# Performance work log

Hardware: AMD Instinct MI355X
Metric: run time of the kernel (lower is better)

The kernel has to match this reference:

```python
import jax, jax.numpy as jnp
import numpy as np

D_MODEL = 768
NUM_HEADS = 12
HEAD_DIM = D_MODEL // NUM_HEADS
THETA = 10000.0
BATCH = 4
SEQ = 2048


def setup_inputs() -> dict:
    key = jax.random.key(0)
    ks = jax.random.split(key, 5)
    scale = 1.0 / np.sqrt(D_MODEL)
    x = jax.random.normal(ks[0], (BATCH, SEQ, D_MODEL), dtype=jnp.float32)
    w_q = jax.random.normal(ks[1], (D_MODEL, D_MODEL), dtype=jnp.float32) * scale
    w_k = jax.random.normal(ks[2], (D_MODEL, D_MODEL), dtype=jnp.float32) * scale
    w_v = jax.random.normal(ks[3], (D_MODEL, D_MODEL), dtype=jnp.float32) * scale
    w_o = jax.random.normal(ks[4], (D_MODEL, D_MODEL), dtype=jnp.float32) * scale
    token_positions = jnp.arange(SEQ, dtype=jnp.int32)
    return {"x": x, "w_q": w_q, "w_k": w_k, "w_v": w_v, "w_o": w_o,
            "token_positions": token_positions}


def _rope(t, positions):
    # t: [b, h, s, d]; rotate even/odd pairs with theta^(-2i/d) frequencies
    d = t.shape[-1]
    inv_freq = THETA ** (-jnp.arange(0, d, 2, dtype=jnp.float32) / d)  # [d/2]
    ang = positions.astype(jnp.float32)[:, None] * inv_freq[None, :]   # [s, d/2]
    cos, sin = jnp.cos(ang), jnp.sin(ang)
    t_even, t_odd = t[..., 0::2], t[..., 1::2]
    out_even = t_even * cos - t_odd * sin
    out_odd = t_even * sin + t_odd * cos
    return jnp.stack([out_even, out_odd], axis=-1).reshape(t.shape)


def reference(x, w_q, w_k, w_v, w_o, token_positions):
    b, s, d = x.shape
    # fused QKV projection: x @ concat(Wq, Wk, Wv).T
    w_qkv = jnp.concatenate([w_q, w_k, w_v], axis=0)  # [3d, d]
    qkv = x @ w_qkv.T                                  # [b, s, 3d]
    q, k, v = jnp.split(qkv, 3, axis=-1)
    def split_heads(t):
        return t.reshape(b, s, NUM_HEADS, HEAD_DIM).transpose(0, 2, 1, 3)  # [b,h,s,dh]
    q, k, v = split_heads(q), split_heads(k), split_heads(v)
    q = _rope(q, token_positions)
    k = _rope(k, token_positions)
    scores = jnp.einsum('bhqd,bhkd->bhqk', q, k) / np.sqrt(HEAD_DIM)  # [b,h,s,s]
    causal = jnp.tril(jnp.ones((s, s), dtype=bool))
    scores = jnp.where(causal, scores, -jnp.inf)
    attn = jax.nn.softmax(scores, axis=-1)
    out = jnp.einsum('bhqk,bhkd->bhqd', attn, v)       # [b,h,s,dh]
    out = out.transpose(0, 2, 1, 3).reshape(b, s, d)   # [b,s,d]
    return out @ w_o.T
```

## Files before the change

kernel.cpp:

```cpp
#include <hip/hip_runtime.h>
#include <hip/hip_bf16.h>
#include <math.h>

#define L2E 1.44269504088896340736f

using f32x4  = __attribute__((ext_vector_type(4))) float;
using f32x16 = __attribute__((ext_vector_type(16))) float;
using bf16x8 = __attribute__((ext_vector_type(8))) short;

static __device__ __forceinline__ float b2f(unsigned short u) {
  union { unsigned u; float f; } v; v.u = ((unsigned)u) << 16; return v.f;
}
static __device__ __forceinline__ unsigned short f2b(float f) {
  union { float f; unsigned u; } v; v.f = f;
  unsigned r = (v.u + 0x7FFFu + ((v.u >> 16) & 1u)) >> 16;
  return (unsigned short)r;
}
static __device__ __forceinline__ unsigned cvtpk(float a, float b) {
  unsigned r;
  asm("v_cvt_pk_bf16_f32 %0, %1, %2" : "=v"(r) : "v"(a), "v"(b));
  return r;
}
static __device__ __forceinline__ void plswap(unsigned& a, unsigned& b) {
#if __has_builtin(__builtin_amdgcn_permlane32_swap)
  typedef unsigned u32x2 __attribute__((ext_vector_type(2)));
  u32x2 r = __builtin_amdgcn_permlane32_swap(a, b, false, false);
  a = r[0]; b = r[1];
#else
  unsigned as = (unsigned)__shfl_xor((int)a, 32, 64);
  unsigned bs = (unsigned)__shfl_xor((int)b, 32, 64);
  bool lo = (threadIdx.x & 32) == 0;
  unsigned na = lo ? a : bs;
  unsigned nb = lo ? as : b;
  a = na; b = nb;
#endif
}

__global__ void cvt_kernel(const float* __restrict__ src,
                           unsigned short* __restrict__ dst, int n4) {
  int i = blockIdx.x * blockDim.x + threadIdx.x;
  int stride = gridDim.x * blockDim.x;
  for (; i < n4; i += stride) {
    float4 v = ((const float4*)src)[i];
    ushort4 o;
    o.x = f2b(v.x); o.y = f2b(v.y); o.z = f2b(v.z); o.w = f2b(v.w);
    ((ushort4*)dst)[i] = o;
  }
}

__global__ void rope_table_kernel(const int* __restrict__ pos,
                                  float2* __restrict__ tab) {
  int t = blockIdx.x * blockDim.x + threadIdx.x;
  int s = t >> 5, j = t & 31;
  double p = (double)pos[s];
  double freq = pow(10000.0, -(double)(2 * j) / 64.0);
  double ang = p * freq;
  tab[t] = make_float2((float)cos(ang), (float)sin(ang));
}

template <typename OUT>
__global__ __launch_bounds__(256) void gemm_nt(const unsigned short* __restrict__ A,
                                               const unsigned short* __restrict__ B,
                                               OUT* __restrict__ C,
                                               int M, int N, int K) {
  __shared__ unsigned short As[128 * 64];
  __shared__ unsigned short Bs[128 * 64];
  const int t = threadIdx.x;
  const int lane = t & 63;
  const int row_l = lane & 15;
  const int grp = lane >> 4;
  const int wave = t >> 6;
  const int wm = (wave >> 1) * 64;
  const int wn = (wave & 1) * 64;
  const int m0 = blockIdx.y * 128;
  const int n0 = blockIdx.x * 128;

  f32x4 acc[4][4];
#pragma unroll
  for (int i = 0; i < 4; ++i)
#pragma unroll
    for (int j = 0; j < 4; ++j) acc[i][j] = (f32x4){0.f, 0.f, 0.f, 0.f};

  const int srow = t >> 3;
  const int scolb = (t & 7) * 16;
  const size_t lda = (size_t)K * 2;
  const char* Ab = (const char*)A + (size_t)m0 * lda + scolb;
  const char* Bb = (const char*)B + (size_t)n0 * lda + scolb;

  for (int k0 = 0; k0 < K; k0 += 64) {
#pragma unroll
    for (int it = 0; it < 4; ++it) {
      int row = it * 32 + srow;
      const char* ga = Ab + (size_t)row * lda + (size_t)k0 * 2;
      const char* gb = Bb + (size_t)row * lda + (size_t)k0 * 2;
      __builtin_amdgcn_global_load_lds(
          (const __attribute__((address_space(1))) unsigned*)ga,
          (__attribute__((address_space(3))) unsigned*)((char*)As + it * 4096 + t * 16),
          16, 0, 0);
      __builtin_amdgcn_global_load_lds(
          (const __attribute__((address_space(1))) unsigned*)gb,
          (__attribute__((address_space(3))) unsigned*)((char*)Bs + it * 4096 + t * 16),
          16, 0, 0);
    }
    __syncthreads();
#pragma unroll
    for (int kk = 0; kk < 2; ++kk) {
      bf16x8 a[4], b[4];
#pragma unroll
      for (int i = 0; i < 4; ++i)
        a[i] = *(const bf16x8*)&As[(wm + 16 * i + row_l) * 64 + kk * 32 + grp * 8];
#pragma unroll
      for (int j = 0; j < 4; ++j)
        b[j] = *(const bf16x8*)&Bs[(wn + 16 * j + row_l) * 64 + kk * 32 + grp * 8];
#pragma unroll
      for (int i = 0; i < 4; ++i)
#pragma unroll
        for (int j = 0; j < 4; ++j)
          acc[i][j] = __builtin_amdgcn_mfma_f32_16x16x32_bf16(a[i], b[j], acc[i][j], 0, 0, 0);
    }
    __syncthreads();
  }
#pragma unroll
  for (int i = 0; i < 4; ++i)
#pragma unroll
    for (int j = 0; j < 4; ++j)
#pragma unroll
      for (int r = 0; r < 4; ++r) {
        int rowg = m0 + wm + 16 * i + grp * 4 + r;
        int colg = n0 + wn + 16 * j + row_l;
        float v = acc[i][j][r];
        if constexpr (sizeof(OUT) == 2) {
          C[(size_t)rowg * N + colg] = (OUT)f2b(v);
        } else {
          C[(size_t)rowg * N + colg] = v;
        }
      }
}

__global__ __launch_bounds__(256) void split_rope_kernel(
    const unsigned short* __restrict__ qkv, const float2* __restrict__ tab,
    unsigned short* __restrict__ Qo, unsigned short* __restrict__ Ko) {
  int idx = blockIdx.x * 256 + threadIdx.x;
  int d2 = idx & 31;
  int h = (idx >> 5) % 12;
  int m = idx / 384;
  int b = m >> 11, s = m & 2047;
  const unsigned short* rowp = qkv + (size_t)m * 2304;
  int c0 = h * 64 + 2 * d2;
  float qe = b2f(rowp[c0]),       qo = b2f(rowp[c0 + 1]);
  float ke = b2f(rowp[768 + c0]), ko = b2f(rowp[768 + c0 + 1]);
  float2 cs = tab[s * 32 + d2];
  float c = cs.x, sn = cs.y;
  float qre = (qe * c - qo * sn) * 0.125f;
  float qro = (qe * sn + qo * c) * 0.125f;
  float kre = ke * c - ko * sn;
  float kro = ke * sn + ko * c;
  size_t bh = (size_t)(b * 12 + h);
  size_t qoff = (bh * 2048 + s) * 64 + 2 * d2;
  ushort2 qv; qv.x = f2b(qre); qv.y = f2b(qro);
  *(ushort2*)&Qo[qoff] = qv;
  ushort2 kv; kv.x = f2b(kre); kv.y = f2b(kro);
  *(ushort2*)&Ko[qoff] = kv;
}

__global__ __launch_bounds__(256) void vtrans_kernel(
    const unsigned short* __restrict__ qkv, unsigned short* __restrict__ Vt) {
  __shared__ unsigned short T[64][72];
  const int bh = blockIdx.x;
  const int st = blockIdx.y;
  const int b = bh / 12, h = bh - b * 12;
  const int t = threadIdx.x;
  const size_t m0 = (size_t)b * 2048 + st * 64;
  const int row = t >> 2;
  const int cp = t & 3;
  const unsigned short* src = qkv + (m0 + row) * 2304 + 1536 + h * 64 + cp * 16;
  *(bf16x8*)&T[row][cp * 16]     = *(const bf16x8*)src;
  *(bf16x8*)&T[row][cp * 16 + 8] = *(const bf16x8*)(src + 8);
  __syncthreads();
  const int d = t >> 2;
  const int sp = t & 3;
  unsigned short tmp[16];
#pragma unroll
  for (int i = 0; i < 16; ++i) tmp[i] = T[sp * 16 + i][d];
  unsigned short* dst = &Vt[((size_t)bh * 64 + d) * 2048 + st * 64 + sp * 16];
  *(bf16x8*)dst       = *(bf16x8*)&tmp[0];
  *(bf16x8*)(dst + 8) = *(bf16x8*)&tmp[8];
}

__global__ __launch_bounds__(256) void attn_kernel(
    const unsigned short* __restrict__ Q, const unsigned short* __restrict__ Kc,
    const unsigned short* __restrict__ Vt, unsigned short* __restrict__ Ao) {
  __shared__ unsigned short Ol[4][32][72];
  const int lane = threadIdx.x & 63;
  const int wave = threadIdx.x >> 6;
  const int ql = lane & 31;
  const int hi = lane >> 5;
  const int bh = blockIdx.x;
  const int q0 = blockIdx.y * 128 + wave * 32;
  const size_t base = (size_t)bh * 2048 * 64;
  const size_t vbase = (size_t)bh * 64 * 2048;

  bf16x8 bq[4];
  const unsigned short* qp = &Q[base + (size_t)(q0 + ql) * 64 + hi * 8];
#pragma unroll
  for (int kk = 0; kk < 4; ++kk) bq[kk] = *(const bf16x8*)(qp + kk * 16);

  f32x16 o0, o1;
#pragma unroll
  for (int i = 0; i < 16; ++i) { o0[i] = 0.f; o1[i] = 0.f; }
  float m = -3.0e38f, lsum = 0.f;

  const int nfull = q0 >> 5;
  for (int kt = 0; kt <= nfull; ++kt) {
    const int k0 = kt << 5;
    f32x16 s;
#pragma unroll
    for (int i = 0; i < 16; ++i) s[i] = 0.f;
    const unsigned short* kp = &Kc[base + (size_t)(k0 + ql) * 64 + hi * 8];
#pragma unroll
    for (int kk = 0; kk < 4; ++kk) {
      bf16x8 ak = *(const bf16x8*)(kp + kk * 16);
      s = __builtin_amdgcn_mfma_f32_32x32x16_bf16(ak, bq[kk], s, 0, 0, 0);
    }
    if (kt == nfull) {
#pragma unroll
      for (int r = 0; r < 16; ++r) {
        int key = k0 + (r & 3) + ((r >> 2) << 3) + (hi << 2);
        if (key > q0 + ql) s[r] = -3.0e38f;
      }
    }
    float tm = fmaxf(fmaxf(fmaxf(s[0], s[1]), fmaxf(s[2], s[3])),
                     fmaxf(fmaxf(s[4], s[5]), fmaxf(s[6], s[7])));
    tm = fmaxf(tm, fmaxf(fmaxf(fmaxf(s[8], s[9]), fmaxf(s[10], s[11])),
                         fmaxf(fmaxf(s[12], s[13]), fmaxf(s[14], s[15]))));
    tm = fmaxf(tm, __shfl_xor(tm, 32, 64));
    float nm = fmaxf(m, tm);
    float al = exp2f((m - nm) * L2E);
    m = nm;
    float mL2 = m * L2E;
    float p[16];
    float rs = 0.f;
#pragma unroll
    for (int r = 0; r < 16; ++r) {
      float pv = exp2f(s[r] * L2E - mL2);
      p[r] = pv;
      rs += pv;
    }
    lsum = lsum * al + rs;
    o0 *= al;
    o1 *= al;
    unsigned w0 = cvtpk(p[0], p[1]),   w2 = cvtpk(p[4], p[5]);
    unsigned w1 = cvtpk(p[2], p[3]),   w3 = cvtpk(p[6], p[7]);
    unsigned w4 = cvtpk(p[8], p[9]),   w6 = cvtpk(p[12], p[13]);
    unsigned w5 = cvtpk(p[10], p[11]), w7 = cvtpk(p[14], p[15]);
    plswap(w0, w2);
    plswap(w1, w3);
    plswap(w4, w6);
    plswap(w5, w7);
    union { unsigned u[4]; bf16x8 v; } pb0, pb1;
    pb0.u[0] = w0; pb0.u[1] = w1; pb0.u[2] = w2; pb0.u[3] = w3;
    pb1.u[0] = w4; pb1.u[1] = w5; pb1.u[2] = w6; pb1.u[3] = w7;
    const unsigned short* vp0 = &Vt[vbase + (size_t)ql * 2048 + k0 + hi * 8];
    const unsigned short* vp1 = vp0 + (size_t)32 * 2048;
    bf16x8 av00 = *(const bf16x8*)vp0;
    bf16x8 av01 = *(const bf16x8*)(vp0 + 16);
    bf16x8 av10 = *(const bf16x8*)vp1;
    bf16x8 av11 = *(const bf16x8*)(vp1 + 16);
    o0 = __builtin_amdgcn_mfma_f32_32x32x16_bf16(av00, pb0.v, o0, 0, 0, 0);
    o0 = __builtin_amdgcn_mfma_f32_32x32x16_bf16(av01, pb1.v, o0, 0, 0, 0);
    o1 = __builtin_amdgcn_mfma_f32_32x32x16_bf16(av10, pb0.v, o1, 0, 0, 0);
    o1 = __builtin_amdgcn_mfma_f32_32x32x16_bf16(av11, pb1.v, o1, 0, 0, 0);
  }
  float lt = lsum + __shfl_xor(lsum, 32, 64);
  float linv = 1.0f / lt;
  unsigned short (*Ow)[72] = Ol[wave];
#pragma unroll
  for (int r = 0; r < 16; ++r) {
    int d = (r & 3) + ((r >> 2) << 3) + (hi << 2);
    Ow[ql][d]      = f2b(o0[r] * linv);
    Ow[ql][32 + d] = f2b(o1[r] * linv);
  }
  const int b = bh / 12, h = bh - b * 12;
  const int qr = lane >> 1, hf = lane & 1;
  unsigned short* orow = &Ao[((size_t)(b * 2048 + q0 + qr)) * 768 + h * 64 + hf * 32];
#pragma unroll
  for (int jj = 0; jj < 4; ++jj)
    *(bf16x8*)(orow + jj * 8) = *(bf16x8*)&Ow[qr][hf * 32 + jj * 8];
}

extern "C" void kernel_launch(void* const* d_in, const int* in_sizes, int n_in,
                              void* d_out, int out_size, void* d_ws, size_t ws_size,
                              hipStream_t stream) {
  const float* x  = (const float*)d_in[0];
  const float* wq = (const float*)d_in[1];
  const float* wk = (const float*)d_in[2];
  const float* wv = (const float*)d_in[3];
  const float* wo = (const float*)d_in[4];
  const int* tpos = (const int*)d_in[5];
  float* out = (float*)d_out;

  char* ws = (char*)d_ws;
  unsigned short* xb   = (unsigned short*)(ws + 0);
  unsigned short* wqkv = (unsigned short*)(ws + 12582912);
  unsigned short* wob  = (unsigned short*)(ws + 16121856);
  float2*         tab  = (float2*)(ws + 17301504);
  unsigned short* qkv  = (unsigned short*)(ws + 17825792);
  unsigned short* Qb   = (unsigned short*)(ws + 55574528);
  unsigned short* Kb   = (unsigned short*)(ws + 68157440);
  unsigned short* Vtb  = (unsigned short*)(ws + 80740352);
  unsigned short* aout = xb;

  cvt_kernel<<<2048, 256, 0, stream>>>(x, xb, 8192 * 768 / 4);
  cvt_kernel<<<576, 256, 0, stream>>>(wq, wqkv, 768 * 768 / 4);
  cvt_kernel<<<576, 256, 0, stream>>>(wk, wqkv + 589824, 768 * 768 / 4);
  cvt_kernel<<<576, 256, 0, stream>>>(wv, wqkv + 1179648, 768 * 768 / 4);
  cvt_kernel<<<576, 256, 0, stream>>>(wo, wob, 768 * 768 / 4);
  rope_table_kernel<<<256, 256, 0, stream>>>(tpos, tab);
  gemm_nt<unsigned short><<<dim3(18, 64), 256, 0, stream>>>(xb, wqkv, qkv, 8192, 2304, 768);
  split_rope_kernel<<<12288, 256, 0, stream>>>(qkv, tab, Qb, Kb);
  vtrans_kernel<<<dim3(48, 32), 256, 0, stream>>>(qkv, Vtb);
  attn_kernel<<<dim3(48, 16), 256, 0, stream>>>(Qb, Kb, Vtb, aout);
  gemm_nt<float><<<dim3(6, 64), 256, 0, stream>>>(aout, wob, out, 8192, 768, 768);
}
```

Baseline: 318.3 us.

## Split attention keys across waves per 32-query block and merge in LDS

Each attention block now owns a single 32-query tile, and its four waves divide the key tiles among themselves in stride 4. The per-wave partial max, sum and output are merged through shared memory before writing. The grid grows from 16 to 64 query blocks and is issued heaviest-first, which aims to balance causal work and raise occupancy. Three weight conversion launches are also merged into one. The cost is an extra LDS reduction and a barrier in every block, and Q/K/V tiles are no longer shared across the waves of a block.

After: 296.4 us. -6.9%, faster.

```diff
diff --git a/kernel.cpp b/kernel.cpp
--- a/kernel.cpp
+++ b/kernel.cpp
@@ -46,6 +46,18 @@
     o.x = f2b(v.x); o.y = f2b(v.y); o.z = f2b(v.z); o.w = f2b(v.w);
     ((ushort4*)dst)[i] = o;
   }
+}
+
+__global__ void wcvt_kernel(const float* __restrict__ wq, const float* __restrict__ wk,
+                            const float* __restrict__ wv, unsigned short* __restrict__ dst) {
+  int i = blockIdx.x * blockDim.x + threadIdx.x;
+  int which = i / 147456;
+  int sub = i - which * 147456;
+  const float* src = which == 0 ? wq : (which == 1 ? wk : wv);
+  float4 v = ((const float4*)src)[sub];
+  ushort4 o;
+  o.x = f2b(v.x); o.y = f2b(v.y); o.z = f2b(v.z); o.w = f2b(v.w);
+  ((ushort4*)dst)[i] = o;
 }
 
 __global__ void rope_table_kernel(const int* __restrict__ pos,
@@ -190,15 +202,17 @@
 __global__ __launch_bounds__(256) void attn_kernel(
     const unsigned short* __restrict__ Q, const unsigned short* __restrict__ Kc,
     const unsigned short* __restrict__ Vt, unsigned short* __restrict__ Ao) {
-  __shared__ unsigned short Ol[4][32][72];
+  __shared__ float Ob[4][32][68];
+  __shared__ float Ml[4][32];
+  __shared__ float Ll[4][32];
   const int lane = threadIdx.x & 63;
   const int wave = threadIdx.x >> 6;
   const int ql = lane & 31;
   const int hi = lane >> 5;
   const int bh = blockIdx.x;
-  const int q0 = blockIdx.y * 128 + wave * 32;
+  const int p = (int)gridDim.y - 1 - (int)blockIdx.y;
+  const int q0 = p << 5;
   const size_t base = (size_t)bh * 2048 * 64;
-  const size_t vbase = (size_t)bh * 64 * 2048;
 
   bf16x8 bq[4];
   const unsigned short* qp = &Q[base + (size_t)(q0 + ql) * 64 + hi * 8];
@@ -210,8 +224,7 @@
   for (int i = 0; i < 16; ++i) { o0[i] = 0.f; o1[i] = 0.f; }
   float m = -3.0e38f, lsum = 0.f;
 
-  const int nfull = q0 >> 5;
-  for (int kt = 0; kt <= nfull; ++kt) {
+  for (int kt = wave; kt <= p; kt += 4) {
     const int k0 = kt << 5;
     f32x16 s;
 #pragma unroll
@@ -222,7 +235,7 @@
       bf16x8 ak = *(const bf16x8*)(kp + kk * 16);
       s = __builtin_amdgcn_mfma_f32_32x32x16_bf16(ak, bq[kk], s, 0, 0, 0);
     }
-    if (kt == nfull) {
+    if (kt == p) {
 #pragma unroll
       for (int r = 0; r < 16; ++r) {
         int key = k0 + (r & 3) + ((r >> 2) << 3) + (hi << 2);
@@ -238,21 +251,21 @@
     float al = exp2f((m - nm) * L2E);
     m = nm;
     float mL2 = m * L2E;
-    float p[16];
+    float pr[16];
     float rs = 0.f;
 #pragma unroll
     for (int r = 0; r < 16; ++r) {
       float pv = exp2f(s[r] * L2E - mL2);
-      p[r] = pv;
+      pr[r] = pv;
       rs += pv;
     }
     lsum = lsum * al + rs;
     o0 *= al;
     o1 *= al;
-    unsigned w0 = cvtpk(p[0], p[1]),   w2 = cvtpk(p[4], p[5]);
-    unsigned w1 = cvtpk(p[2], p[3]),   w3 = cvtpk(p[6], p[7]);
-    unsigned w4 = cvtpk(p[8], p[9]),   w6 = cvtpk(p[12], p[13]);
-    unsigned w5 = cvtpk(p[10], p[11]), w7 = cvtpk(p[14], p[15]);
+    unsigned w0 = cvtpk(pr[0], pr[1]),   w2 = cvtpk(pr[4], pr[5]);
+    unsigned w1 = cvtpk(pr[2], pr[3]),   w3 = cvtpk(pr[6], pr[7]);
+    unsigned w4 = cvtpk(pr[8], pr[9]),   w6 = cvtpk(pr[12], pr[13]);
+    unsigned w5 = cvtpk(pr[10], pr[11]), w7 = cvtpk(pr[14], pr[15]);
     plswap(w0, w2);
     plswap(w1, w3);
     plswap(w4, w6);
@@ -260,7 +273,7 @@
     union { unsigned u[4]; bf16x8 v; } pb0, pb1;
     pb0.u[0] = w0; pb0.u[1] = w1; pb0.u[2] = w2; pb0.u[3] = w3;
     pb1.u[0] = w4; pb1.u[1] = w5; pb1.u[2] = w6; pb1.u[3] = w7;
-    const unsigned short* vp0 = &Vt[vbase + (size_t)ql * 2048 + k0 + hi * 8];
+    const unsigned short* vp0 = &Vt[base + (size_t)ql * 2048 + k0 + hi * 8];
     const unsigned short* vp1 = vp0 + (size_t)32 * 2048;
     bf16x8 av00 = *(const bf16x8*)vp0;
     bf16x8 av01 = *(const bf16x8*)(vp0 + 16);
@@ -272,20 +285,33 @@
     o1 = __builtin_amdgcn_mfma_f32_32x32x16_bf16(av11, pb1.v, o1, 0, 0, 0);
   }
   float lt = lsum + __shfl_xor(lsum, 32, 64);
-  float linv = 1.0f / lt;
-  unsigned short (*Ow)[72] = Ol[wave];
+  if (hi == 0) { Ml[wave][ql] = m; Ll[wave][ql] = lt; }
 #pragma unroll
   for (int r = 0; r < 16; ++r) {
     int d = (r & 3) + ((r >> 2) << 3) + (hi << 2);
-    Ow[ql][d]      = f2b(o0[r] * linv);
-    Ow[ql][32 + d] = f2b(o1[r] * linv);
+    Ob[wave][ql][d]      = o0[r];
+    Ob[wave][ql][32 + d] = o1[r];
+  }
+  __syncthreads();
+  const int qr = (wave << 3) + (lane >> 3);
+  const int db = (lane & 7) << 3;
+  float m0 = Ml[0][qr], m1 = Ml[1][qr], m2 = Ml[2][qr], m3 = Ml[3][qr];
+  float ms = fmaxf(fmaxf(m0, m1), fmaxf(m2, m3));
+  float sc0 = exp2f((m0 - ms) * L2E);
+  float sc1 = exp2f((m1 - ms) * L2E);
+  float sc2 = exp2f((m2 - ms) * L2E);
+  float sc3 = exp2f((m3 - ms) * L2E);
+  float lstar = sc0 * Ll[0][qr] + sc1 * Ll[1][qr] + sc2 * Ll[2][qr] + sc3 * Ll[3][qr];
+  float linv = 1.0f / lstar;
+  unsigned short ov[8];
+#pragma unroll
+  for (int j = 0; j < 8; ++j) {
+    float a = sc0 * Ob[0][qr][db + j] + sc1 * Ob[1][qr][db + j]
+            + sc2 * Ob[2][qr][db + j] + sc3 * Ob[3][qr][db + j];
+    ov[j] = f2b(a * linv);
   }
   const int b = bh / 12, h = bh - b * 12;
-  const int qr = lane >> 1, hf = lane & 1;
-  unsigned short* orow = &Ao[((size_t)(b * 2048 + q0 + qr)) * 768 + h * 64 + hf * 32];
-#pragma unroll
-  for (int jj = 0; jj < 4; ++jj)
-    *(bf16x8*)(orow + jj * 8) = *(bf16x8*)&Ow[qr][hf * 32 + jj * 8];
+  *(bf16x8*)&Ao[((size_t)(b * 2048 + q0 + qr)) * 768 + h * 64 + db] = *(bf16x8*)ov;
 }
 
 extern "C" void kernel_launch(void* const* d_in, const int* in_sizes, int n_in,
@@ -311,14 +337,12 @@
   unsigned short* aout = xb;
 
   cvt_kernel<<<2048, 256, 0, stream>>>(x, xb, 8192 * 768 / 4);
-  cvt_kernel<<<576, 256, 0, stream>>>(wq, wqkv, 768 * 768 / 4);
-  cvt_kernel<<<576, 256, 0, stream>>>(wk, wqkv + 589824, 768 * 768 / 4);
-  cvt_kernel<<<576, 256, 0, stream>>>(wv, wqkv + 1179648, 768 * 768 / 4);
+  wcvt_kernel<<<1728, 256, 0, stream>>>(wq, wk, wv, wqkv);
   cvt_kernel<<<576, 256, 0, stream>>>(wo, wob, 768 * 768 / 4);
   rope_table_kernel<<<256, 256, 0, stream>>>(tpos, tab);
   gemm_nt<unsigned short><<<dim3(18, 64), 256, 0, stream>>>(xb, wqkv, qkv, 8192, 2304, 768);
   split_rope_kernel<<<12288, 256, 0, stream>>>(qkv, tab, Qb, Kb);
   vtrans_kernel<<<dim3(48, 32), 256, 0, stream>>>(qkv, Vtb);
-  attn_kernel<<<dim3(48, 16), 256, 0, stream>>>(Qb, Kb, Vtb, aout);
+  attn_kernel<<<dim3(48, 64), 256, 0, stream>>>(Qb, Kb, Vtb, aout);
   gemm_nt<float><<<dim3(6, 64), 256, 0, stream>>>(aout, wob, out, 8192, 768, 768);
 }
```
